# Performance work log

Hardware: AMD Instinct MI355X
Metric: run time of the kernel (lower is better)

## Reference

```python
import jax, jax.numpy as jnp
import numpy as np

IN_FEATURES = 1024
OUT_FEATURES = 1024
NUM_EXPERTS = 4
RANK = 16  # total_rank=64 / num_experts=4, rem=0 -> equal ranks
NETWORK_ALPHA = 64.0


def setup_inputs() -> dict:
    key = jax.random.key(0)
    k1, k2, k3, k4 = jax.random.split(key, 4)
    hidden_states = jax.random.normal(k1, (4, 4096, IN_FEATURES), dtype=jnp.float32)
    alpha = jax.random.uniform(k2, (4, NUM_EXPERTS), dtype=jnp.float32)
    # down: K Linear(in, r) weights, each [r, in], init std=1/r (as in torch init)
    down_w = jax.random.normal(k3, (NUM_EXPERTS, RANK, IN_FEATURES), dtype=jnp.float32) / RANK
    # up: K Linear(r, out) weights, each [out, r]. Torch inits these to zero,
    # which would make the output identically zero; use small random values so
    # the reference exercises the full math.
    up_w = jax.random.normal(k4, (NUM_EXPERTS, OUT_FEATURES, RANK), dtype=jnp.float32) * 0.02
    return {"hidden_states": hidden_states, "alpha": alpha, "down_w": down_w, "up_w": up_w}


def reference(hidden_states, alpha, down_w, up_w):
    # hidden_states: [B, N, D]; alpha: [B, K]
    # down_w: [K, r, D]; up_w: [K, out, r]
    scale = NETWORK_ALPHA / RANK  # network_alpha / rank_per_expert (equal ranks)
    # per-expert down projection: [B, K, N, r]
    low = jnp.einsum('bnd,krd->bknr', hidden_states, down_w)
    # up projection + scale + alpha-weighted sum over experts, fused: [B, N, out]
    out = jnp.einsum('bknr,kor,bk->bno', low, up_w, alpha) * scale
    return out
```

## Files before the change

### kernel.cpp

```cpp
#include <hip/hip_runtime.h>

namespace {

typedef short  bf16x8 __attribute__((ext_vector_type(8)));
typedef float  f32x4  __attribute__((ext_vector_type(4)));

constexpr int D = 1024;
constexpr int O = 1024;

__device__ __forceinline__ short f2bf(float f) {
    unsigned u = __builtin_bit_cast(unsigned, f);
    u += 0x7fffu + ((u >> 16) & 1u);
    return (short)(u >> 16);
}

__device__ __forceinline__ bf16x8 cvt8(const float4 a, const float4 b) {
    bf16x8 v;
    v[0] = f2bf(a.x); v[1] = f2bf(a.y); v[2] = f2bf(a.z); v[3] = f2bf(a.w);
    v[4] = f2bf(b.x); v[5] = f2bf(b.y); v[6] = f2bf(b.z); v[7] = f2bf(b.w);
    return v;
}

struct StageRegs { float4 a[4]; float4 b[4]; };

__device__ __forceinline__ void issue_dw(const float* __restrict__ dw, int c, int t,
                                         StageRegs& r) {
#pragma unroll
    for (int i = 0; i < 4; ++i) {
        const int e = i * 512 + t, kr = e >> 5, cc = e & 31;
        const float* sp = dw + (size_t)kr * D + c * 256 + cc * 8;
        r.a[i] = *reinterpret_cast<const float4*>(sp);
        r.b[i] = *reinterpret_cast<const float4*>(sp + 4);
    }
}
__device__ __forceinline__ void write_p1(short* buf, int t, const StageRegs& r) {
#pragma unroll
    for (int i = 0; i < 4; ++i) {
        const int e = i * 512 + t, kr = e >> 5, cc = e & 31;
        *reinterpret_cast<bf16x8*>(&buf[kr * 264 + cc * 8]) = cvt8(r.a[i], r.b[i]);
    }
}
__device__ __forceinline__ void issue_uw(const float* __restrict__ uw, int oc, int t,
                                         StageRegs& r) {
#pragma unroll
    for (int i = 0; i < 4; ++i) {
        const int e = i * 512 + t, o = e >> 3, cc = e & 7;
        const int k = cc >> 1, r0 = (cc & 1) * 8;
        const float* sp = uw + (size_t)k * 16384 + (size_t)(oc * 256 + o) * 16 + r0;
        r.a[i] = *reinterpret_cast<const float4*>(sp);
        r.b[i] = *reinterpret_cast<const float4*>(sp + 4);
    }
}
__device__ __forceinline__ void write_p2(short* buf, int t, const StageRegs& r) {
#pragma unroll
    for (int i = 0; i < 4; ++i) {
        const int e = i * 512 + t, o = e >> 3, cc = e & 7;
        *reinterpret_cast<bf16x8*>(&buf[o * 72 + cc * 8]) = cvt8(r.a[i], r.b[i]);
    }
}

__device__ __forceinline__ void compute_p1(const short* __restrict__ buf,
                                           const float* __restrict__ ap,
                                           int fr, int kh, int kg, f32x4* acc) {
#pragma unroll
    for (int ks = 0; ks < 4; ++ks) {
        const float4 a0 = *reinterpret_cast<const float4*>(ap + ks * 32);
        const float4 a1 = *reinterpret_cast<const float4*>(ap + ks * 32 + 4);
        const bf16x8 av = cvt8(a0, a1);
#pragma unroll
        for (int nt = 0; nt < 4; ++nt) {
            const bf16x8 bv = *reinterpret_cast<const bf16x8*>(
                &buf[(nt * 16 + fr) * 264 + kh * 128 + ks * 32 + kg]);
            acc[nt] = __builtin_amdgcn_mfma_f32_16x16x32_bf16(av, bv, acc[nt], 0, 0, 0);
        }
    }
}

__device__ __forceinline__ void compute_p2(const short* __restrict__ buf,
                                           const bf16x8 pa0, const bf16x8 pa1,
                                           float* __restrict__ op,
                                           int oc, int fr, int kg, int kh) {
#pragma unroll
    for (int ntl = 0; ntl < 8; ++ntl) {
        const int nt = kh * 8 + ntl;
        const bf16x8 b0 = *reinterpret_cast<const bf16x8*>(&buf[(nt * 16 + fr) * 72 + kg]);
        const bf16x8 b1 = *reinterpret_cast<const bf16x8*>(&buf[(nt * 16 + fr) * 72 + 32 + kg]);
        f32x4 c2 = (f32x4){0.f, 0.f, 0.f, 0.f};
        c2 = __builtin_amdgcn_mfma_f32_16x16x32_bf16(pa0, b0, c2, 0, 0, 0);
        c2 = __builtin_amdgcn_mfma_f32_16x16x32_bf16(pa1, b1, c2, 0, 0, 0);
#pragma unroll
        for (int j = 0; j < 4; ++j)
            op[(size_t)j * O + oc * 256 + nt * 16 + fr] = c2[j];
    }
}

__global__ void __launch_bounds__(512) lora_mfma_k(
        const float* __restrict__ hs,
        const float* __restrict__ alpha,
        const float* __restrict__ dw,
        const float* __restrict__ uw,
        float* __restrict__ out) {
    __shared__ __align__(16) short bs[2][18432];
    __shared__ __align__(16) short lowb[4][16][72];
    __shared__ float pacc[4][16][64];

    const int t    = threadIdx.x;
    const int w    = t >> 6;
    const int lane = t & 63;
    const int rt   = w >> 1;
    const int kh   = w & 1;
    const int fr   = lane & 15;
    const int kgi  = lane >> 4;
    const int kg   = kgi * 8;
    const int rowblk = blockIdx.x * 64;
    const int b      = rowblk >> 12;
    const int myrow  = rowblk + rt * 16 + fr;
    const float* apb = hs + (size_t)myrow * D + kh * 128 + kg;

    StageRegs rg;
    f32x4 acc[4];
#pragma unroll
    for (int nt = 0; nt < 4; ++nt) acc[nt] = (f32x4){0.f, 0.f, 0.f, 0.f};

    issue_dw(dw, 0, t, rg);
    write_p1(&bs[0][0], t, rg);
    __syncthreads();

#pragma unroll
    for (int c = 0; c < 3; ++c) {
        issue_dw(dw, c + 1, t, rg);
        compute_p1(&bs[c & 1][0], apb + c * 256, fr, kh, kg, acc);
        write_p1(&bs[(c + 1) & 1][0], t, rg);
        __syncthreads();
    }
    issue_uw(uw, 0, t, rg);
    compute_p1(&bs[1][0], apb + 3 * 256, fr, kh, kg, acc);
    write_p2(&bs[0][0], t, rg);
    __syncthreads();

    if (kh) {
#pragma unroll
        for (int nt = 0; nt < 4; ++nt)
#pragma unroll
            for (int j = 0; j < 4; ++j)
                pacc[rt][nt * 4 + j][lane] = acc[nt][j];
    }
    __syncthreads();
    if (!kh) {
#pragma unroll
        for (int nt = 0; nt < 4; ++nt) {
            const float sc = alpha[b * 4 + nt] * 4.0f;
#pragma unroll
            for (int j = 0; j < 4; ++j) {
                const float v = (acc[nt][j] + pacc[rt][nt * 4 + j][lane]) * sc;
                lowb[rt][kgi * 4 + j][nt * 16 + fr] = f2bf(v);
            }
        }
    }
    __syncthreads();

    const bf16x8 pa0 = *reinterpret_cast<const bf16x8*>(&lowb[rt][fr][kg]);
    const bf16x8 pa1 = *reinterpret_cast<const bf16x8*>(&lowb[rt][fr][32 + kg]);
    float* op = out + (size_t)(rowblk + rt * 16 + kgi * 4) * O;

#pragma unroll
    for (int oc = 0; oc < 3; ++oc) {
        issue_uw(uw, oc + 1, t, rg);
        compute_p2(&bs[oc & 1][0], pa0, pa1, op, oc, fr, kg, kh);
        write_p2(&bs[(oc + 1) & 1][0], t, rg);
        __syncthreads();
    }
    compute_p2(&bs[1][0], pa0, pa1, op, 3, fr, kg, kh);
}

}

extern "C" void kernel_launch(void* const* d_in, const int* in_sizes, int n_in,
                              void* d_out, int out_size, void* d_ws, size_t ws_size,
                              hipStream_t stream) {
    const float* hs    = (const float*)d_in[0];
    const float* alpha = (const float*)d_in[1];
    const float* dw    = (const float*)d_in[2];
    const float* uw    = (const float*)d_in[3];
    float* outp = (float*)d_out;

    hipLaunchKernelGGL(lora_mfma_k, dim3(256), dim3(512), 0, stream,
                       hs, alpha, dw, uw, outp);
}
```

Baseline: 32.60 us.

## Keep up-projection weights in registers and register-prefetch activations in down phase

Each wave now loads its 128-column slice of the up-projection weights straight from global memory into registers (converted to bf16) at kernel start. The output phase therefore runs without LDS staging or barriers, looping over all four row tiles. The down-projection loop also prefetches the next chunk of hidden-state activations into registers one step ahead, alongside the down-weight prefetch. This removes the up-weight LDS pipeline and its syncs, and hides activation load latency. In exchange it raises register pressure (16 bf16x8 weights plus 8 float4 prefetch registers per thread), which may lower occupancy.

New measurement: 32.74 us. Within noise of the previous version (+0.4%).

```diff
diff --git a/kernel.cpp b/kernel.cpp
--- a/kernel.cpp
+++ b/kernel.cpp
@@ -21,6 +21,10 @@
     return v;
 }
 
+__device__ __forceinline__ float4 ld4(const float* p) {
+    return *reinterpret_cast<const float4*>(p);
+}
+
 struct StageRegs { float4 a[4]; float4 b[4]; };
 
 __device__ __forceinline__ void issue_dw(const float* __restrict__ dw, int c, int t,
@@ -29,8 +33,8 @@
     for (int i = 0; i < 4; ++i) {
         const int e = i * 512 + t, kr = e >> 5, cc = e & 31;
         const float* sp = dw + (size_t)kr * D + c * 256 + cc * 8;
-        r.a[i] = *reinterpret_cast<const float4*>(sp);
-        r.b[i] = *reinterpret_cast<const float4*>(sp + 4);
+        r.a[i] = ld4(sp);
+        r.b[i] = ld4(sp + 4);
     }
 }
 __device__ __forceinline__ void write_p1(short* buf, int t, const StageRegs& r) {
@@ -40,59 +44,6 @@
         *reinterpret_cast<bf16x8*>(&buf[kr * 264 + cc * 8]) = cvt8(r.a[i], r.b[i]);
     }
 }
-__device__ __forceinline__ void issue_uw(const float* __restrict__ uw, int oc, int t,
-                                         StageRegs& r) {
-#pragma unroll
-    for (int i = 0; i < 4; ++i) {
-        const int e = i * 512 + t, o = e >> 3, cc = e & 7;
-        const int k = cc >> 1, r0 = (cc & 1) * 8;
-        const float* sp = uw + (size_t)k * 16384 + (size_t)(oc * 256 + o) * 16 + r0;
-        r.a[i] = *reinterpret_cast<const float4*>(sp);
-        r.b[i] = *reinterpret_cast<const float4*>(sp + 4);
-    }
-}
-__device__ __forceinline__ void write_p2(short* buf, int t, const StageRegs& r) {
-#pragma unroll
-    for (int i = 0; i < 4; ++i) {
-        const int e = i * 512 + t, o = e >> 3, cc = e & 7;
-        *reinterpret_cast<bf16x8*>(&buf[o * 72 + cc * 8]) = cvt8(r.a[i], r.b[i]);
-    }
-}
-
-__device__ __forceinline__ void compute_p1(const short* __restrict__ buf,
-                                           const float* __restrict__ ap,
-                                           int fr, int kh, int kg, f32x4* acc) {
-#pragma unroll
-    for (int ks = 0; ks < 4; ++ks) {
-        const float4 a0 = *reinterpret_cast<const float4*>(ap + ks * 32);
-        const float4 a1 = *reinterpret_cast<const float4*>(ap + ks * 32 + 4);
-        const bf16x8 av = cvt8(a0, a1);
-#pragma unroll
-        for (int nt = 0; nt < 4; ++nt) {
-            const bf16x8 bv = *reinterpret_cast<const bf16x8*>(
-                &buf[(nt * 16 + fr) * 264 + kh * 128 + ks * 32 + kg]);
-            acc[nt] = __builtin_amdgcn_mfma_f32_16x16x32_bf16(av, bv, acc[nt], 0, 0, 0);
-        }
-    }
-}
-
-__device__ __forceinline__ void compute_p2(const short* __restrict__ buf,
-                                           const bf16x8 pa0, const bf16x8 pa1,
-                                           float* __restrict__ op,
-                                           int oc, int fr, int kg, int kh) {
-#pragma unroll
-    for (int ntl = 0; ntl < 8; ++ntl) {
-        const int nt = kh * 8 + ntl;
-        const bf16x8 b0 = *reinterpret_cast<const bf16x8*>(&buf[(nt * 16 + fr) * 72 + kg]);
-        const bf16x8 b1 = *reinterpret_cast<const bf16x8*>(&buf[(nt * 16 + fr) * 72 + 32 + kg]);
-        f32x4 c2 = (f32x4){0.f, 0.f, 0.f, 0.f};
-        c2 = __builtin_amdgcn_mfma_f32_16x16x32_bf16(pa0, b0, c2, 0, 0, 0);
-        c2 = __builtin_amdgcn_mfma_f32_16x16x32_bf16(pa1, b1, c2, 0, 0, 0);
-#pragma unroll
-        for (int j = 0; j < 4; ++j)
-            op[(size_t)j * O + oc * 256 + nt * 16 + fr] = c2[j];
-    }
-}
 
 __global__ void __launch_bounds__(512) lora_mfma_k(
         const float* __restrict__ hs,
@@ -100,43 +51,83 @@
         const float* __restrict__ dw,
         const float* __restrict__ uw,
         float* __restrict__ out) {
-    __shared__ __align__(16) short bs[2][18432];
+    __shared__ __align__(16) short bs[2][64 * 264];
     __shared__ __align__(16) short lowb[4][16][72];
     __shared__ float pacc[4][16][64];
 
     const int t    = threadIdx.x;
     const int w    = t >> 6;
     const int lane = t & 63;
-    const int rt   = w >> 1;
-    const int kh   = w & 1;
     const int fr   = lane & 15;
     const int kgi  = lane >> 4;
     const int kg   = kgi * 8;
+    const int rt   = w >> 1;
+    const int kh   = w & 1;
     const int rowblk = blockIdx.x * 64;
     const int b      = rowblk >> 12;
     const int myrow  = rowblk + rt * 16 + fr;
     const float* apb = hs + (size_t)myrow * D + kh * 128 + kg;
 
     StageRegs rg;
+    issue_dw(dw, 0, t, rg);
+
+    float4 pf[8];
+#pragma unroll
+    for (int ks = 0; ks < 4; ++ks) {
+        pf[2 * ks]     = ld4(apb + ks * 32);
+        pf[2 * ks + 1] = ld4(apb + ks * 32 + 4);
+    }
+
+    bf16x8 wreg[16];
+#pragma unroll
+    for (int nt2l = 0; nt2l < 8; ++nt2l)
+#pragma unroll
+        for (int h = 0; h < 2; ++h) {
+            const int kr0 = h * 32 + kg;
+            const int k   = kr0 >> 4;
+            const int r0  = kr0 & 15;
+            const float* sp = uw + (size_t)k * 16384
+                                 + (size_t)(w * 128 + nt2l * 16 + fr) * 16 + r0;
+            wreg[nt2l * 2 + h] = cvt8(ld4(sp), ld4(sp + 4));
+        }
+
+    write_p1(&bs[0][0], t, rg);
+    __syncthreads();
+
     f32x4 acc[4];
 #pragma unroll
     for (int nt = 0; nt < 4; ++nt) acc[nt] = (f32x4){0.f, 0.f, 0.f, 0.f};
 
-    issue_dw(dw, 0, t, rg);
-    write_p1(&bs[0][0], t, rg);
-    __syncthreads();
+#pragma unroll
+    for (int c = 0; c < 4; ++c) {
+        bf16x8 av[4];
+#pragma unroll
+        for (int ks = 0; ks < 4; ++ks) av[ks] = cvt8(pf[2 * ks], pf[2 * ks + 1]);
+
+        if (c < 3) {
+            const float* ap = apb + (c + 1) * 256;
+#pragma unroll
+            for (int ks = 0; ks < 4; ++ks) {
+                pf[2 * ks]     = ld4(ap + ks * 32);
+                pf[2 * ks + 1] = ld4(ap + ks * 32 + 4);
+            }
+            issue_dw(dw, c + 1, t, rg);
+        }
 
 #pragma unroll
-    for (int c = 0; c < 3; ++c) {
-        issue_dw(dw, c + 1, t, rg);
-        compute_p1(&bs[c & 1][0], apb + c * 256, fr, kh, kg, acc);
-        write_p1(&bs[(c + 1) & 1][0], t, rg);
-        __syncthreads();
+        for (int ks = 0; ks < 4; ++ks)
+#pragma unroll
+            for (int nt = 0; nt < 4; ++nt) {
+                const bf16x8 bv = *reinterpret_cast<const bf16x8*>(
+                    &bs[c & 1][(nt * 16 + fr) * 264 + kh * 128 + ks * 32 + kg]);
+                acc[nt] = __builtin_amdgcn_mfma_f32_16x16x32_bf16(av[ks], bv, acc[nt], 0, 0, 0);
+            }
+
+        if (c < 3) {
+            write_p1(&bs[(c + 1) & 1][0], t, rg);
+            __syncthreads();
+        }
     }
-    issue_uw(uw, 0, t, rg);
-    compute_p1(&bs[1][0], apb + 3 * 256, fr, kh, kg, acc);
-    write_p2(&bs[0][0], t, rg);
-    __syncthreads();
 
     if (kh) {
 #pragma unroll
@@ -159,18 +150,21 @@
     }
     __syncthreads();
 
-    const bf16x8 pa0 = *reinterpret_cast<const bf16x8*>(&lowb[rt][fr][kg]);
-    const bf16x8 pa1 = *reinterpret_cast<const bf16x8*>(&lowb[rt][fr][32 + kg]);
-    float* op = out + (size_t)(rowblk + rt * 16 + kgi * 4) * O;
-
 #pragma unroll
-    for (int oc = 0; oc < 3; ++oc) {
-        issue_uw(uw, oc + 1, t, rg);
-        compute_p2(&bs[oc & 1][0], pa0, pa1, op, oc, fr, kg, kh);
-        write_p2(&bs[(oc + 1) & 1][0], t, rg);
-        __syncthreads();
+    for (int rt2 = 0; rt2 < 4; ++rt2) {
+        const bf16x8 pa0 = *reinterpret_cast<const bf16x8*>(&lowb[rt2][fr][kg]);
+        const bf16x8 pa1 = *reinterpret_cast<const bf16x8*>(&lowb[rt2][fr][32 + kg]);
+        float* op = out + (size_t)(rowblk + rt2 * 16 + kgi * 4) * O + w * 128;
+#pragma unroll
+        for (int nt2l = 0; nt2l < 8; ++nt2l) {
+            f32x4 c2 = (f32x4){0.f, 0.f, 0.f, 0.f};
+            c2 = __builtin_amdgcn_mfma_f32_16x16x32_bf16(pa0, wreg[nt2l * 2],     c2, 0, 0, 0);
+            c2 = __builtin_amdgcn_mfma_f32_16x16x32_bf16(pa1, wreg[nt2l * 2 + 1], c2, 0, 0, 0);
+#pragma unroll
+            for (int j = 0; j < 4; ++j)
+                op[(size_t)j * O + nt2l * 16 + fr] = c2[j];
+        }
     }
-    compute_p2(&bs[1][0], pa0, pa1, op, 3, fr, kg, kh);
 }
 
 }
```
